# Performance work log

Measured on AMD Instinct MI355X. Metric: run time of the kernel, lower is better.

Reference implementation:

```python
import jax, jax.numpy as jnp
import numpy as np

N_NODES = 10000
N_EDGES = 640000
N_GRAPHS = 64
D = 128
N_BLOCKS = 2
NEG_SLOPE = 0.01  # F.leaky_relu default


def setup_inputs() -> dict:
    key = jax.random.key(0)
    ks = jax.random.split(key, 9)
    x = jax.random.normal(ks[0], (N_NODES, D), dtype=jnp.float32)
    edge_src = jax.random.randint(ks[1], (N_EDGES,), 0, N_NODES, dtype=jnp.int32)
    edge_dst = jax.random.randint(ks[2], (N_EDGES,), 0, N_NODES, dtype=jnp.int32)
    graph_ids = jnp.sort(jax.random.randint(ks[3], (N_NODES,), 0, N_GRAPHS, dtype=jnp.int32))
    s = 1.414 / np.sqrt(D)  # xavier-normal-ish scale
    Wfc = jax.random.normal(ks[4], (N_BLOCKS, D, D), dtype=jnp.float32) * s
    bfc = jnp.zeros((N_BLOCKS, D), dtype=jnp.float32)
    wl = jax.random.normal(ks[5], (N_BLOCKS, D), dtype=jnp.float32) * s
    wr = jax.random.normal(ks[6], (N_BLOCKS, D), dtype=jnp.float32) * s
    Wres = jax.random.normal(ks[7], (N_BLOCKS, D, D), dtype=jnp.float32) * s
    return {"x": x, "edge_src": edge_src, "edge_dst": edge_dst, "graph_ids": graph_ids,
            "Wfc": Wfc, "bfc": bfc, "wl": wl, "wr": wr, "Wres": Wres}


def _gat_block(x, edge_src, edge_dst, Wfc_b, bfc_b, wl_b, wr_b, Wres_b):
    # node projections: nn.Linear -> x @ W^T + b
    feat = x @ Wfc_b.T + bfc_b                       # [N, D]
    a_self = feat @ wl_b                              # [N] self_a (dst side)
    a_nb = feat @ wr_b                                # [N] attn  (src side)
    # per-edge score: leaky_relu(self_a[dst] + attn[src])
    s = a_self[edge_dst] + a_nb[edge_src]             # [E]
    s = jnp.where(s >= 0, s, NEG_SLOPE * s)
    # segment softmax over incoming edges of each dst node
    m = jax.ops.segment_max(s, edge_dst, num_segments=N_NODES)   # [N]
    e = jnp.exp(s - m[edge_dst])                                  # [E]
    denom = jax.ops.segment_sum(e, edge_dst, num_segments=N_NODES)
    w = e / denom[edge_dst]                                       # [E]
    # attention-weighted neighbor aggregation
    accum = jax.ops.segment_sum(w[:, None] * feat[edge_src], edge_dst,
                                num_segments=N_NODES)             # [N, D]
    # residual (in_size == out_size -> res_fc, no bias), then relu
    out = accum + x @ Wres_b.T
    return jax.nn.relu(out)


def reference(x, edge_src, edge_dst, graph_ids, Wfc, bfc, wl, wr, Wres):
    blocks = [
        _gat_block(x, edge_src, edge_dst, Wfc[b], bfc[b], wl[b], wr[b], Wres[b])
        for b in range(N_BLOCKS)
    ]
    h = jnp.concatenate(blocks, axis=1)               # mode='concat' -> [N, 2*D]
    # dgl.sum_nodes: per-graph sum pooling
    phis = jax.ops.segment_sum(h, graph_ids, num_segments=N_GRAPHS)  # [G, 2*D]
    return h, phis
```

## Files before the change

kernel.cpp:

```cpp
#include <hip/hip_runtime.h>
#include <hip/hip_bf16.h>
#include <math.h>

#define N_NODES 10000
#define N_EDGES 640000
#define N_GRAPHS 64
#define DIM 128
#define NEG_SLOPE 0.01f
#define NB_CSR 128
#define EDGES_PER_BLK (N_EDGES / NB_CSR)

typedef __attribute__((ext_vector_type(8))) short bf16x8;
typedef __attribute__((ext_vector_type(4))) float f32x4;


__device__ __forceinline__ unsigned short f2bf(float f) {
    __hip_bfloat16 h = __float2bfloat16(f);
    return *reinterpret_cast<unsigned short*>(&h);
}

__global__ __launch_bounds__(256) void gemm_mfma(
    const float* __restrict__ x, const float* __restrict__ Wfc,
    const float* __restrict__ bfc, const float* __restrict__ Wres,
    const float* __restrict__ wl, const float* __restrict__ wr,
    unsigned short* __restrict__ resid_b16, unsigned short* __restrict__ feat_b16,
    float* __restrict__ a_self, float* __restrict__ a_nb) {
    const int which = blockIdx.y & 1;
    const int b = blockIdx.y >> 1;
    const float* __restrict__ W = (which ? Wres : Wfc) + b * DIM * DIM;
    const int n0 = blockIdx.x * 64;
    const int t = threadIdx.x;

    __shared__ unsigned short xs[64][136];
    __shared__ unsigned short wsh[128][136];

    {
        const int r = t >> 2, qq = t & 3;
        const int n = n0 + r;
        ushort4* drow = reinterpret_cast<ushort4*>(&xs[r][qq * 32]);
        if (n < N_NODES) {
            const float4* p = reinterpret_cast<const float4*>(x + (size_t)n * DIM + qq * 32);
#pragma unroll
            for (int i = 0; i < 8; ++i) {
                float4 v = p[i];
                ushort4 u;
                u.x = f2bf(v.x); u.y = f2bf(v.y); u.z = f2bf(v.z); u.w = f2bf(v.w);
                drow[i] = u;
            }
        } else {
            ushort4 z = {0, 0, 0, 0};
#pragma unroll
            for (int i = 0; i < 8; ++i) drow[i] = z;
        }
    }
    {
        const int rw = t >> 1, hh = t & 1;
        const float4* p = reinterpret_cast<const float4*>(W + (size_t)rw * DIM + hh * 64);
        ushort4* drow = reinterpret_cast<ushort4*>(&wsh[rw][hh * 64]);
#pragma unroll
        for (int i = 0; i < 16; ++i) {
            float4 v = p[i];
            ushort4 u;
            u.x = f2bf(v.x); u.y = f2bf(v.y); u.z = f2bf(v.z); u.w = f2bf(v.w);
            drow[i] = u;
        }
    }
    __syncthreads();

    const int wave = t >> 6, lane = t & 63;
    const int quad = lane >> 4, jc = lane & 15;
    const int m0 = wave * 16;

    bf16x8 af[4];
#pragma unroll
    for (int ks = 0; ks < 4; ++ks)
        af[ks] = *reinterpret_cast<const bf16x8*>(&xs[m0 + jc][ks * 32 + quad * 8]);

    f32x4 accs[8];
    float ps[4] = {0.f, 0.f, 0.f, 0.f}, pr[4] = {0.f, 0.f, 0.f, 0.f};
#pragma unroll
    for (int jt = 0; jt < 8; ++jt) {
        f32x4 acc = {0.f, 0.f, 0.f, 0.f};
#pragma unroll
        for (int ks = 0; ks < 4; ++ks) {
            bf16x8 bfr = *reinterpret_cast<const bf16x8*>(
                &wsh[jt * 16 + jc][ks * 32 + quad * 8]);
            acc = __builtin_amdgcn_mfma_f32_16x16x32_bf16(af[ks], bfr, acc, 0, 0, 0);
        }
        if (!which) {
            float bias = bfc[b * DIM + jt * 16 + jc];
            acc[0] += bias; acc[1] += bias; acc[2] += bias; acc[3] += bias;
            float wlv = wl[b * DIM + jt * 16 + jc];
            float wrv = wr[b * DIM + jt * 16 + jc];
#pragma unroll
            for (int r2 = 0; r2 < 4; ++r2) { ps[r2] += acc[r2] * wlv; pr[r2] += acc[r2] * wrv; }
        }
        accs[jt] = acc;
    }

    __syncthreads();

    if (!which) {
#pragma unroll
        for (int off = 8; off > 0; off >>= 1) {
#pragma unroll
            for (int r2 = 0; r2 < 4; ++r2) {
                ps[r2] += __shfl_xor(ps[r2], off, 64);
                pr[r2] += __shfl_xor(pr[r2], off, 64);
            }
        }
        if (jc == 0) {
#pragma unroll
            for (int r2 = 0; r2 < 4; ++r2) {
                int n = n0 + m0 + quad * 4 + r2;
                if (n < N_NODES) {
                    a_self[b * N_NODES + n] = ps[r2];
                    a_nb[b * N_NODES + n] = pr[r2];
                }
            }
        }
    }

    unsigned short* dst_buf = which ? resid_b16 : feat_b16;
#pragma unroll
    for (int jt = 0; jt < 8; ++jt)
#pragma unroll
        for (int r2 = 0; r2 < 4; ++r2)
            xs[m0 + quad * 4 + r2][jt * 16 + jc] = f2bf(accs[jt][r2]);
    __syncthreads();
    {
        const int r = t >> 2, qq = t & 3;
        const int n = n0 + r;
        if (n < N_NODES) {
            uint4* dst = reinterpret_cast<uint4*>(
                dst_buf + ((size_t)b * N_NODES + n) * DIM + qq * 32);
            const uint4* srcp = reinterpret_cast<const uint4*>(&xs[r][qq * 32]);
#pragma unroll
            for (int i = 0; i < 4; ++i) dst[i] = srcp[i];
        }
    }
}

__global__ __launch_bounds__(1024) void csr_hist(const int4* __restrict__ edst4,
                                                 unsigned short* __restrict__ bh16) {
    __shared__ int hist[N_NODES];
    const int blk = blockIdx.x;
    const int t = threadIdx.x;
    for (int n = t; n < N_NODES; n += 1024) hist[n] = 0;
    __syncthreads();
    const int base4 = blk * (EDGES_PER_BLK / 4);
    for (int i = t; i < EDGES_PER_BLK / 4; i += 1024) {
        int4 d = edst4[base4 + i];
        atomicAdd(&hist[d.x], 1);
        atomicAdd(&hist[d.y], 1);
        atomicAdd(&hist[d.z], 1);
        atomicAdd(&hist[d.w], 1);
    }
    __syncthreads();
    unsigned short* dst = bh16 + (size_t)blk * N_NODES;
    for (int n = t; n < N_NODES; n += 1024) dst[n] = (unsigned short)hist[n];
}

__device__ __forceinline__ unsigned int pack16(int a, int b) {
    return (a & 0xffff) | (b << 16);
}

__global__ __launch_bounds__(256) void csr_node_scan(unsigned short* __restrict__ bh16,
                                                     int* __restrict__ deg) {
    int n8 = blockIdx.x * 256 + threadIdx.x;
    if (n8 >= N_NODES / 8) return;
    int run[8] = {0, 0, 0, 0, 0, 0, 0, 0};
    for (int blk = 0; blk < NB_CSR; ++blk) {
        uint4* p = reinterpret_cast<uint4*>(bh16 + (size_t)blk * N_NODES) + n8;
        uint4 v = *p;
        uint4 o;
        o.x = pack16(run[0], run[1]); o.y = pack16(run[2], run[3]);
        o.z = pack16(run[4], run[5]); o.w = pack16(run[6], run[7]);
        *p = o;
        run[0] += v.x & 0xffff; run[1] += v.x >> 16;
        run[2] += v.y & 0xffff; run[3] += v.y >> 16;
        run[4] += v.z & 0xffff; run[5] += v.z >> 16;
        run[6] += v.w & 0xffff; run[7] += v.w >> 16;
    }
    int4* d4 = reinterpret_cast<int4*>(deg) + n8 * 2;
    d4[0] = make_int4(run[0], run[1], run[2], run[3]);
    d4[1] = make_int4(run[4], run[5], run[6], run[7]);
}

__global__ __launch_bounds__(1024) void scan_deg(const int* __restrict__ deg,
                                                 int* __restrict__ rowptr,
                                                 float* __restrict__ phis) {
    __shared__ int sdata[1024];
    const int tid = threadIdx.x;
    for (int i = tid; i < N_GRAPHS * 2 * DIM; i += 1024) phis[i] = 0.f;

    const int base = tid * 10;
    int cnt = N_NODES - base;
    if (cnt < 0) cnt = 0;
    if (cnt > 10) cnt = 10;
    int local[10];
    int s = 0;
    for (int i = 0; i < cnt; ++i) { local[i] = s; s += deg[base + i]; }
    sdata[tid] = s;
    __syncthreads();
    for (int off = 1; off < 1024; off <<= 1) {
        int v = 0;
        if (tid >= off) v = sdata[tid - off];
        __syncthreads();
        if (tid >= off) sdata[tid] += v;
        __syncthreads();
    }
    int pre = (tid == 0) ? 0 : sdata[tid - 1];
    for (int i = 0; i < cnt; ++i) rowptr[base + i] = pre + local[i];
    if (tid == 1023) rowptr[N_NODES] = sdata[1023];
}

__global__ __launch_bounds__(1024) void csr_scatter(
    const int4* __restrict__ esrc4, const int4* __restrict__ edst4,
    const int* __restrict__ rowptr, const unsigned short* __restrict__ bh16,
    const float* __restrict__ a_self, const float* __restrict__ a_nb,
    int2* __restrict__ csr_sw) {
    __shared__ int cur[N_NODES];
    const int blk = blockIdx.x;
    const int t = threadIdx.x;
    const unsigned short* boff = bh16 + (size_t)blk * N_NODES;
    for (int n = t; n < N_NODES; n += 1024) cur[n] = rowptr[n] + (int)boff[n];
    __syncthreads();
    const float* __restrict__ asl0 = a_self;
    const float* __restrict__ asl1 = a_self + N_NODES;
    const float* __restrict__ anb0 = a_nb;
    const float* __restrict__ anb1 = a_nb + N_NODES;
    int2* __restrict__ sw0 = csr_sw;
    int2* __restrict__ sw1 = csr_sw + N_EDGES;
    const int base4 = blk * (EDGES_PER_BLK / 4);
    for (int i = t; i < EDGES_PER_BLK / 4; i += 1024) {
        int4 s = esrc4[base4 + i];
        int4 d = edst4[base4 + i];
#pragma unroll
        for (int k = 0; k < 4; ++k) {
            int se = (&s.x)[k];
            int de = (&d.x)[k];
            int pos = atomicAdd(&cur[de], 1);
            float t0 = asl0[de] + anb0[se];
            t0 = (t0 >= 0.f) ? t0 : NEG_SLOPE * t0;
            float t1 = asl1[de] + anb1[se];
            t1 = (t1 >= 0.f) ? t1 : NEG_SLOPE * t1;
            sw0[pos] = make_int2(se, __float_as_int(__expf(t0)));
            sw1[pos] = make_int2(se, __float_as_int(__expf(t1)));
        }
    }
}

__global__ __launch_bounds__(256) void aggregate(
    const unsigned short* __restrict__ feat_b16,
    const unsigned short* __restrict__ resid_b16,
    const int2* __restrict__ csr_sw, const int* __restrict__ rowptr,
    float* __restrict__ out) {
    const int wave = threadIdx.x >> 6;
    const int lane = threadIdx.x & 63;
    const int n = blockIdx.x * 4 + wave;
    const int b = blockIdx.y;
    const int q = lane >> 4;
    const int l16 = lane & 15;
    const int start = rowptr[n];
    const int end = rowptr[n + 1];

    const int2* __restrict__ swb = csr_sw + (size_t)b * N_EDGES;
    const uint4* __restrict__ fb =
        reinterpret_cast<const uint4*>(feat_b16 + (size_t)b * N_NODES * DIM);

    float acc[8];
#pragma unroll
    for (int k = 0; k < 8; ++k) acc[k] = 0.f;
    float dpart = 0.f;

    for (int c = start; c < end; c += 64) {
        int j = c + lane;
        float e = 0.f;
        int src = 0;
        if (j < end) {
            int2 sw = swb[j];
            src = sw.x;
            e = __int_as_float(sw.y);
        }
        dpart += e;
        int cnt = end - c;
        if (cnt > 64) cnt = 64;
        int iters = (cnt + 3) >> 2;

        float w0 = __shfl(e, q, 64);
        int s0 = __shfl(src, q, 64);
        uint4 f0 = fb[(size_t)s0 * 16 + l16];

        for (int i2 = 0; i2 < iters - 1; ++i2) {
            int idx = (i2 + 1) * 4 + q;
            float w1 = __shfl(e, idx, 64);
            int s1 = __shfl(src, idx, 64);
            uint4 f1 = fb[(size_t)s1 * 16 + l16];
#pragma unroll
            for (int k = 0; k < 4; ++k) {
                unsigned int u = (&f0.x)[k];
                float lo = __uint_as_float(u << 16);
                float hi = __uint_as_float(u & 0xffff0000u);
                acc[2 * k]     += w0 * lo;
                acc[2 * k + 1] += w0 * hi;
            }
            w0 = w1; f0 = f1;
        }
#pragma unroll
        for (int k = 0; k < 4; ++k) {
            unsigned int u = (&f0.x)[k];
            float lo = __uint_as_float(u << 16);
            float hi = __uint_as_float(u & 0xffff0000u);
            acc[2 * k]     += w0 * lo;
            acc[2 * k + 1] += w0 * hi;
        }
    }

#pragma unroll
    for (int k = 0; k < 8; ++k) {
        acc[k] += __shfl_xor(acc[k], 16, 64);
        acc[k] += __shfl_xor(acc[k], 32, 64);
    }
    float denom = dpart;
#pragma unroll
    for (int off = 32; off > 0; off >>= 1) denom += __shfl_xor(denom, off, 64);

    if (q == 0) {
        float inv = (end > start) ? 1.f / denom : 0.f;
        uint4 rb = reinterpret_cast<const uint4*>(
            resid_b16 + ((size_t)b * N_NODES + n) * DIM)[l16];
        float4 o0, o1;
        {
            unsigned int u = rb.x;
            o0.x = fmaxf(acc[0] * inv + __uint_as_float(u << 16), 0.f);
            o0.y = fmaxf(acc[1] * inv + __uint_as_float(u & 0xffff0000u), 0.f);
            u = rb.y;
            o0.z = fmaxf(acc[2] * inv + __uint_as_float(u << 16), 0.f);
            o0.w = fmaxf(acc[3] * inv + __uint_as_float(u & 0xffff0000u), 0.f);
            u = rb.z;
            o1.x = fmaxf(acc[4] * inv + __uint_as_float(u << 16), 0.f);
            o1.y = fmaxf(acc[5] * inv + __uint_as_float(u & 0xffff0000u), 0.f);
            u = rb.w;
            o1.z = fmaxf(acc[6] * inv + __uint_as_float(u << 16), 0.f);
            o1.w = fmaxf(acc[7] * inv + __uint_as_float(u & 0xffff0000u), 0.f);
        }
        float4* po = reinterpret_cast<float4*>(out + (size_t)n * (2 * DIM) + b * DIM);
        po[l16 * 2] = o0;
        po[l16 * 2 + 1] = o1;
    }
}

__device__ int lower_bound_dev(const int* __restrict__ a, int n, int key) {
    int lo = 0, hi = n;
    while (lo < hi) {
        int mid = (lo + hi) >> 1;
        if (a[mid] < key) lo = mid + 1;
        else hi = mid;
    }
    return lo;
}

__global__ __launch_bounds__(256) void pool_graphs(
    const float* __restrict__ h, const int* __restrict__ gids,
    float* __restrict__ phis) {
    const int g = blockIdx.x;
    const int chunk = blockIdx.y;
    const int tid = threadIdx.x;
    int lo = lower_bound_dev(gids, N_NODES, g);
    int hi = lower_bound_dev(gids, N_NODES, g + 1);
    float acc = 0.f;
    for (int n = lo + chunk; n < hi; n += 16) acc += h[(size_t)n * (2 * DIM) + tid];
    if (acc != 0.f) atomicAdd(&phis[(size_t)g * (2 * DIM) + tid], acc);
}

extern "C" void kernel_launch(void* const* d_in, const int* in_sizes, int n_in,
                              void* d_out, int out_size, void* d_ws, size_t ws_size,
                              hipStream_t stream) {
    const float* x    = (const float*)d_in[0];
    const int* esrc   = (const int*)d_in[1];
    const int* edst   = (const int*)d_in[2];
    const int* gids   = (const int*)d_in[3];
    const float* Wfc  = (const float*)d_in[4];
    const float* bfc  = (const float*)d_in[5];
    const float* wl   = (const float*)d_in[6];
    const float* wr   = (const float*)d_in[7];
    const float* Wres = (const float*)d_in[8];
    float* out = (float*)d_out;

    char* ws = (char*)d_ws;
    float* a_self  = (float*)(ws + 0);
    float* a_nb    = (float*)(ws + 80000);
    int*   deg     = (int*)(ws + 160000);
    int*   rowptr  = (int*)(ws + 200000);
    int2*  csr_sw  = (int2*)(ws + 240032);
    unsigned short* feat_b16  = (unsigned short*)(ws + 10480032);
    unsigned short* resid_b16 = (unsigned short*)(ws + 15600032);
    unsigned short* bh16      = (unsigned short*)(ws + 20720032);

    float* phis = out + (size_t)N_NODES * 2 * DIM;

    gemm_mfma<<<dim3((N_NODES + 63) / 64, 4), 256, 0, stream>>>(
        x, Wfc, bfc, Wres, wl, wr, resid_b16, feat_b16, a_self, a_nb);

    csr_hist<<<NB_CSR, 1024, 0, stream>>>((const int4*)edst, bh16);
    csr_node_scan<<<(N_NODES / 8 + 255) / 256, 256, 0, stream>>>(bh16, deg);
    scan_deg<<<1, 1024, 0, stream>>>(deg, rowptr, phis);
    csr_scatter<<<NB_CSR, 1024, 0, stream>>>(
        (const int4*)esrc, (const int4*)edst, rowptr, bh16, a_self, a_nb, csr_sw);

    aggregate<<<dim3(2500, 2), 256, 0, stream>>>(
        feat_b16, resid_b16, csr_sw, rowptr, out);
    pool_graphs<<<dim3(N_GRAPHS, 16), 256, 0, stream>>>(out, gids, phis);
}
```

Before: 189.8 us.

## Fuse CSR build into one persistent kernel and compute edge weights in aggregate

Merges the histogram, per-node scan, degree scan and scatter kernels into one 128-block kernel that synchronises through spin-wait grid barriers on a global counter, removing three kernel launches. The scatter now writes only source indices instead of a per-block (src, exp score) pair, so the leaky-relu and exp are recomputed inside aggregate from a_self/a_nb. This shrinks the CSR write and read traffic. Aggregate also gains a two-deep prefetch of feature rows. The grid barrier assumes all 128 blocks of 1024 threads are co-resident, and a memset is added to reset the barrier counter on each call.

```diff
diff --git a/kernel.cpp b/kernel.cpp
--- a/kernel.cpp
+++ b/kernel.cpp
@@ -17,6 +17,102 @@
 __device__ __forceinline__ unsigned short f2bf(float f) {
     __hip_bfloat16 h = __float2bfloat16(f);
     return *reinterpret_cast<unsigned short*>(&h);
+}
+
+__device__ __forceinline__ void grid_barrier(int* __restrict__ bar, int idx) {
+    __syncthreads();
+    if (threadIdx.x == 0) {
+        __threadfence();
+        __hip_atomic_fetch_add(&bar[idx], 1, __ATOMIC_ACQ_REL,
+                               __HIP_MEMORY_SCOPE_AGENT);
+        while (__hip_atomic_load(&bar[idx], __ATOMIC_ACQUIRE,
+                                 __HIP_MEMORY_SCOPE_AGENT) < NB_CSR) {
+            __builtin_amdgcn_s_sleep(8);
+        }
+        __threadfence();
+    }
+    __syncthreads();
+}
+
+__global__ __launch_bounds__(1024) void csr_fused(
+    const int4* __restrict__ esrc4, const int4* __restrict__ edst4,
+    int* __restrict__ bh, int* __restrict__ deg, int* __restrict__ rowptr,
+    int* __restrict__ csr_src, float* __restrict__ phis, int* __restrict__ bar) {
+    __shared__ int lds[N_NODES];
+    __shared__ int sdata[1024];
+    const int blk = blockIdx.x;
+    const int t = threadIdx.x;
+    const int base4 = blk * (EDGES_PER_BLK / 4);
+
+    for (int n = t; n < N_NODES; n += 1024) lds[n] = 0;
+    __syncthreads();
+    for (int i = t; i < EDGES_PER_BLK / 4; i += 1024) {
+        int4 d = edst4[base4 + i];
+        atomicAdd(&lds[d.x], 1);
+        atomicAdd(&lds[d.y], 1);
+        atomicAdd(&lds[d.z], 1);
+        atomicAdd(&lds[d.w], 1);
+    }
+    __syncthreads();
+    {
+        int* dst = bh + (size_t)blk * N_NODES;
+        for (int n = t; n < N_NODES; n += 1024) dst[n] = lds[n];
+    }
+    grid_barrier(bar, 0);
+
+    {
+        int g = blk * 1024 + t;
+        if (g < N_NODES / 4) {
+            int4 run = {0, 0, 0, 0};
+            for (int p = 0; p < NB_CSR; ++p) {
+                int4* pp = reinterpret_cast<int4*>(bh + (size_t)p * N_NODES) + g;
+                int4 v = *pp;
+                *pp = run;
+                run.x += v.x; run.y += v.y; run.z += v.z; run.w += v.w;
+            }
+            reinterpret_cast<int4*>(deg)[g] = run;
+        }
+        int z = g - 3 * 1024;
+        if (z >= 0 && z < N_GRAPHS * 2 * DIM) phis[z] = 0.f;
+    }
+    grid_barrier(bar, 1);
+
+    if (blk == 0) {
+        const int base = t * 10;
+        int cnt = N_NODES - base;
+        if (cnt < 0) cnt = 0;
+        if (cnt > 10) cnt = 10;
+        int local[10];
+        int s = 0;
+        for (int i = 0; i < cnt; ++i) { local[i] = s; s += deg[base + i]; }
+        sdata[t] = s;
+        __syncthreads();
+        for (int off = 1; off < 1024; off <<= 1) {
+            int v = 0;
+            if (t >= off) v = sdata[t - off];
+            __syncthreads();
+            if (t >= off) sdata[t] += v;
+            __syncthreads();
+        }
+        int pre = (t == 0) ? 0 : sdata[t - 1];
+        for (int i = 0; i < cnt; ++i) rowptr[base + i] = pre + local[i];
+        if (t == 1023) rowptr[N_NODES] = sdata[1023];
+    }
+    grid_barrier(bar, 2);
+
+    {
+        const int* boff = bh + (size_t)blk * N_NODES;
+        for (int n = t; n < N_NODES; n += 1024) lds[n] = rowptr[n] + boff[n];
+        __syncthreads();
+        for (int i = t; i < EDGES_PER_BLK / 4; i += 1024) {
+            int4 s = esrc4[base4 + i];
+            int4 d = edst4[base4 + i];
+            csr_src[atomicAdd(&lds[d.x], 1)] = s.x;
+            csr_src[atomicAdd(&lds[d.y], 1)] = s.y;
+            csr_src[atomicAdd(&lds[d.z], 1)] = s.z;
+            csr_src[atomicAdd(&lds[d.w], 1)] = s.w;
+        }
+    }
 }
 
 __global__ __launch_bounds__(256) void gemm_mfma(
@@ -121,7 +217,7 @@
         }
     }
 
-    unsigned short* dst_buf = which ? resid_b16 : feat_b16;
+    unsigned short* __restrict__ dstb = which ? resid_b16 : feat_b16;
 #pragma unroll
     for (int jt = 0; jt < 8; ++jt)
 #pragma unroll
@@ -133,120 +229,10 @@
         const int n = n0 + r;
         if (n < N_NODES) {
             uint4* dst = reinterpret_cast<uint4*>(
-                dst_buf + ((size_t)b * N_NODES + n) * DIM + qq * 32);
+                dstb + ((size_t)b * N_NODES + n) * DIM + qq * 32);
             const uint4* srcp = reinterpret_cast<const uint4*>(&xs[r][qq * 32]);
 #pragma unroll
             for (int i = 0; i < 4; ++i) dst[i] = srcp[i];
-        }
-    }
-}
-
-__global__ __launch_bounds__(1024) void csr_hist(const int4* __restrict__ edst4,
-                                                 unsigned short* __restrict__ bh16) {
-    __shared__ int hist[N_NODES];
-    const int blk = blockIdx.x;
-    const int t = threadIdx.x;
-    for (int n = t; n < N_NODES; n += 1024) hist[n] = 0;
-    __syncthreads();
-    const int base4 = blk * (EDGES_PER_BLK / 4);
-    for (int i = t; i < EDGES_PER_BLK / 4; i += 1024) {
-        int4 d = edst4[base4 + i];
-        atomicAdd(&hist[d.x], 1);
-        atomicAdd(&hist[d.y], 1);
-        atomicAdd(&hist[d.z], 1);
-        atomicAdd(&hist[d.w], 1);
-    }
-    __syncthreads();
-    unsigned short* dst = bh16 + (size_t)blk * N_NODES;
-    for (int n = t; n < N_NODES; n += 1024) dst[n] = (unsigned short)hist[n];
-}
-
-__device__ __forceinline__ unsigned int pack16(int a, int b) {
-    return (a & 0xffff) | (b << 16);
-}
-
-__global__ __launch_bounds__(256) void csr_node_scan(unsigned short* __restrict__ bh16,
-                                                     int* __restrict__ deg) {
-    int n8 = blockIdx.x * 256 + threadIdx.x;
-    if (n8 >= N_NODES / 8) return;
-    int run[8] = {0, 0, 0, 0, 0, 0, 0, 0};
-    for (int blk = 0; blk < NB_CSR; ++blk) {
-        uint4* p = reinterpret_cast<uint4*>(bh16 + (size_t)blk * N_NODES) + n8;
-        uint4 v = *p;
-        uint4 o;
-        o.x = pack16(run[0], run[1]); o.y = pack16(run[2], run[3]);
-        o.z = pack16(run[4], run[5]); o.w = pack16(run[6], run[7]);
-        *p = o;
-        run[0] += v.x & 0xffff; run[1] += v.x >> 16;
-        run[2] += v.y & 0xffff; run[3] += v.y >> 16;
-        run[4] += v.z & 0xffff; run[5] += v.z >> 16;
-        run[6] += v.w & 0xffff; run[7] += v.w >> 16;
-    }
-    int4* d4 = reinterpret_cast<int4*>(deg) + n8 * 2;
-    d4[0] = make_int4(run[0], run[1], run[2], run[3]);
-    d4[1] = make_int4(run[4], run[5], run[6], run[7]);
-}
-
-__global__ __launch_bounds__(1024) void scan_deg(const int* __restrict__ deg,
-                                                 int* __restrict__ rowptr,
-                                                 float* __restrict__ phis) {
-    __shared__ int sdata[1024];
-    const int tid = threadIdx.x;
-    for (int i = tid; i < N_GRAPHS * 2 * DIM; i += 1024) phis[i] = 0.f;
-
-    const int base = tid * 10;
-    int cnt = N_NODES - base;
-    if (cnt < 0) cnt = 0;
-    if (cnt > 10) cnt = 10;
-    int local[10];
-    int s = 0;
-    for (int i = 0; i < cnt; ++i) { local[i] = s; s += deg[base + i]; }
-    sdata[tid] = s;
-    __syncthreads();
-    for (int off = 1; off < 1024; off <<= 1) {
-        int v = 0;
-        if (tid >= off) v = sdata[tid - off];
-        __syncthreads();
-        if (tid >= off) sdata[tid] += v;
-        __syncthreads();
-    }
-    int pre = (tid == 0) ? 0 : sdata[tid - 1];
-    for (int i = 0; i < cnt; ++i) rowptr[base + i] = pre + local[i];
-    if (tid == 1023) rowptr[N_NODES] = sdata[1023];
-}
-
-__global__ __launch_bounds__(1024) void csr_scatter(
-    const int4* __restrict__ esrc4, const int4* __restrict__ edst4,
-    const int* __restrict__ rowptr, const unsigned short* __restrict__ bh16,
-    const float* __restrict__ a_self, const float* __restrict__ a_nb,
-    int2* __restrict__ csr_sw) {
-    __shared__ int cur[N_NODES];
-    const int blk = blockIdx.x;
-    const int t = threadIdx.x;
-    const unsigned short* boff = bh16 + (size_t)blk * N_NODES;
-    for (int n = t; n < N_NODES; n += 1024) cur[n] = rowptr[n] + (int)boff[n];
-    __syncthreads();
-    const float* __restrict__ asl0 = a_self;
-    const float* __restrict__ asl1 = a_self + N_NODES;
-    const float* __restrict__ anb0 = a_nb;
-    const float* __restrict__ anb1 = a_nb + N_NODES;
-    int2* __restrict__ sw0 = csr_sw;
-    int2* __restrict__ sw1 = csr_sw + N_EDGES;
-    const int base4 = blk * (EDGES_PER_BLK / 4);
-    for (int i = t; i < EDGES_PER_BLK / 4; i += 1024) {
-        int4 s = esrc4[base4 + i];
-        int4 d = edst4[base4 + i];
-#pragma unroll
-        for (int k = 0; k < 4; ++k) {
-            int se = (&s.x)[k];
-            int de = (&d.x)[k];
-            int pos = atomicAdd(&cur[de], 1);
-            float t0 = asl0[de] + anb0[se];
-            t0 = (t0 >= 0.f) ? t0 : NEG_SLOPE * t0;
-            float t1 = asl1[de] + anb1[se];
-            t1 = (t1 >= 0.f) ? t1 : NEG_SLOPE * t1;
-            sw0[pos] = make_int2(se, __float_as_int(__expf(t0)));
-            sw1[pos] = make_int2(se, __float_as_int(__expf(t1)));
         }
     }
 }
@@ -254,7 +240,8 @@
 __global__ __launch_bounds__(256) void aggregate(
     const unsigned short* __restrict__ feat_b16,
     const unsigned short* __restrict__ resid_b16,
-    const int2* __restrict__ csr_sw, const int* __restrict__ rowptr,
+    const float* __restrict__ a_self, const float* __restrict__ a_nb,
+    const int* __restrict__ rowptr, const int* __restrict__ csr_src,
     float* __restrict__ out) {
     const int wave = threadIdx.x >> 6;
     const int lane = threadIdx.x & 63;
@@ -265,9 +252,10 @@
     const int start = rowptr[n];
     const int end = rowptr[n + 1];
 
-    const int2* __restrict__ swb = csr_sw + (size_t)b * N_EDGES;
+    const float* __restrict__ anb = a_nb + b * N_NODES;
     const uint4* __restrict__ fb =
         reinterpret_cast<const uint4*>(feat_b16 + (size_t)b * N_NODES * DIM);
+    const float asl = a_self[b * N_NODES + n];
 
     float acc[8];
 #pragma unroll
@@ -279,9 +267,10 @@
         float e = 0.f;
         int src = 0;
         if (j < end) {
-            int2 sw = swb[j];
-            src = sw.x;
-            e = __int_as_float(sw.y);
+            src = csr_src[j];
+            float s = asl + anb[src];
+            s = (s >= 0.f) ? s : NEG_SLOPE * s;
+            e = __expf(s);
         }
         dpart += e;
         int cnt = end - c;
@@ -291,12 +280,23 @@
         float w0 = __shfl(e, q, 64);
         int s0 = __shfl(src, q, 64);
         uint4 f0 = fb[(size_t)s0 * 16 + l16];
-
-        for (int i2 = 0; i2 < iters - 1; ++i2) {
-            int idx = (i2 + 1) * 4 + q;
-            float w1 = __shfl(e, idx, 64);
-            int s1 = __shfl(src, idx, 64);
-            uint4 f1 = fb[(size_t)s1 * 16 + l16];
+        float w1 = 0.f;
+        uint4 f1 = f0;
+        if (iters > 1) {
+            w1 = __shfl(e, 4 + q, 64);
+            int s1 = __shfl(src, 4 + q, 64);
+            f1 = fb[(size_t)s1 * 16 + l16];
+        }
+
+        for (int i2 = 0; i2 < iters; ++i2) {
+            float w2 = 0.f;
+            uint4 f2 = f0;
+            if (i2 + 2 < iters) {
+                int idx = (i2 + 2) * 4 + q;
+                w2 = __shfl(e, idx, 64);
+                int s2 = __shfl(src, idx, 64);
+                f2 = fb[(size_t)s2 * 16 + l16];
+            }
 #pragma unroll
             for (int k = 0; k < 4; ++k) {
                 unsigned int u = (&f0.x)[k];
@@ -306,14 +306,7 @@
                 acc[2 * k + 1] += w0 * hi;
             }
             w0 = w1; f0 = f1;
-        }
-#pragma unroll
-        for (int k = 0; k < 4; ++k) {
-            unsigned int u = (&f0.x)[k];
-            float lo = __uint_as_float(u << 16);
-            float hi = __uint_as_float(u & 0xffff0000u);
-            acc[2 * k]     += w0 * lo;
-            acc[2 * k + 1] += w0 * hi;
+            w1 = w2; f1 = f2;
         }
     }
 
@@ -331,20 +324,18 @@
         uint4 rb = reinterpret_cast<const uint4*>(
             resid_b16 + ((size_t)b * N_NODES + n) * DIM)[l16];
         float4 o0, o1;
-        {
-            unsigned int u = rb.x;
-            o0.x = fmaxf(acc[0] * inv + __uint_as_float(u << 16), 0.f);
-            o0.y = fmaxf(acc[1] * inv + __uint_as_float(u & 0xffff0000u), 0.f);
-            u = rb.y;
-            o0.z = fmaxf(acc[2] * inv + __uint_as_float(u << 16), 0.f);
-            o0.w = fmaxf(acc[3] * inv + __uint_as_float(u & 0xffff0000u), 0.f);
-            u = rb.z;
-            o1.x = fmaxf(acc[4] * inv + __uint_as_float(u << 16), 0.f);
-            o1.y = fmaxf(acc[5] * inv + __uint_as_float(u & 0xffff0000u), 0.f);
-            u = rb.w;
-            o1.z = fmaxf(acc[6] * inv + __uint_as_float(u << 16), 0.f);
-            o1.w = fmaxf(acc[7] * inv + __uint_as_float(u & 0xffff0000u), 0.f);
-        }
+        unsigned int u = rb.x;
+        o0.x = fmaxf(acc[0] * inv + __uint_as_float(u << 16), 0.f);
+        o0.y = fmaxf(acc[1] * inv + __uint_as_float(u & 0xffff0000u), 0.f);
+        u = rb.y;
+        o0.z = fmaxf(acc[2] * inv + __uint_as_float(u << 16), 0.f);
+        o0.w = fmaxf(acc[3] * inv + __uint_as_float(u & 0xffff0000u), 0.f);
+        u = rb.z;
+        o1.x = fmaxf(acc[4] * inv + __uint_as_float(u << 16), 0.f);
+        o1.y = fmaxf(acc[5] * inv + __uint_as_float(u & 0xffff0000u), 0.f);
+        u = rb.w;
+        o1.z = fmaxf(acc[6] * inv + __uint_as_float(u << 16), 0.f);
+        o1.w = fmaxf(acc[7] * inv + __uint_as_float(u & 0xffff0000u), 0.f);
         float4* po = reinterpret_cast<float4*>(out + (size_t)n * (2 * DIM) + b * DIM);
         po[l16 * 2] = o0;
         po[l16 * 2 + 1] = o1;
@@ -389,27 +380,27 @@
     float* out = (float*)d_out;
 
     char* ws = (char*)d_ws;
-    float* a_self  = (float*)(ws + 0);
-    float* a_nb    = (float*)(ws + 80000);
-    int*   deg     = (int*)(ws + 160000);
-    int*   rowptr  = (int*)(ws + 200000);
-    int2*  csr_sw  = (int2*)(ws + 240032);
-    unsigned short* feat_b16  = (unsigned short*)(ws + 10480032);
-    unsigned short* resid_b16 = (unsigned short*)(ws + 15600032);
-    unsigned short* bh16      = (unsigned short*)(ws + 20720032);
+    unsigned short* resid_b16 = (unsigned short*)(ws + 0);
+    float* a_self  = (float*)(ws + 5120000);
+    float* a_nb    = (float*)(ws + 5200000);
+    int*   deg     = (int*)(ws + 5280000);
+    int*   rowptr  = (int*)(ws + 5320000);
+    int*   bar     = (int*)(ws + 5360008);
+    int*   csr_src = (int*)(ws + 5360032);
+    unsigned short* feat_b16 = (unsigned short*)(ws + 7920032);
+    int*   bh      = (int*)(ws + 13040032);
 
     float* phis = out + (size_t)N_NODES * 2 * DIM;
+
+    hipMemsetAsync(bar, 0, 16, stream);
 
     gemm_mfma<<<dim3((N_NODES + 63) / 64, 4), 256, 0, stream>>>(
         x, Wfc, bfc, Wres, wl, wr, resid_b16, feat_b16, a_self, a_nb);
 
-    csr_hist<<<NB_CSR, 1024, 0, stream>>>((const int4*)edst, bh16);
-    csr_node_scan<<<(N_NODES / 8 + 255) / 256, 256, 0, stream>>>(bh16, deg);
-    scan_deg<<<1, 1024, 0, stream>>>(deg, rowptr, phis);
-    csr_scatter<<<NB_CSR, 1024, 0, stream>>>(
-        (const int4*)esrc, (const int4*)edst, rowptr, bh16, a_self, a_nb, csr_sw);
+    csr_fused<<<NB_CSR, 1024, 0, stream>>>(
+        (const int4*)esrc, (const int4*)edst, bh, deg, rowptr, csr_src, phis, bar);
 
     aggregate<<<dim3(2500, 2), 256, 0, stream>>>(
-        feat_b16, resid_b16, csr_sw, rowptr, out);
+        feat_b16, resid_b16, a_self, a_nb, rowptr, csr_src, out);
     pool_graphs<<<dim3(N_GRAPHS, 16), 256, 0, stream>>>(out, gids, phis);
 }
```

Measured after the change: 346.8 us. 82.8% more time.
